# Kernel tuning notes

Hardware: AMD Instinct MI355X
Metric: run time of the kernel (lower is better)

The kernel has to match this reference:

```python
import math
import jax, jax.numpy as jnp
import numpy as np
from jax import lax

# Exact mod-2^32 addition requires float64 accumulation (as the torch code does).
jax.config.update("jax_enable_x64", True)

MD5_K = [int(2 ** 32 * abs(math.sin(i + 1))) & 0xFFFFFFFF for i in range(64)]
MD5_S = [7, 12, 17, 22] * 4 + [5, 9, 14, 20] * 4 + [4, 11, 16, 23] * 4 + [6, 10, 15, 21] * 4
NUM_ROUNDS = 64
NUM_BLOCKS = 2
_XOR_GRAD_SCALE = 0.5

def _int_to_bits(n, width=32):
    return np.array([(n >> i) & 1 for i in range(width)], dtype=np.float32)

K_BITS = np.stack([_int_to_bits(k) for k in MD5_K])          # (64, 32) LSB-first
H0 = _int_to_bits(1732584193)
H1 = _int_to_bits(4023233417)
H2 = _int_to_bits(2562383102)
H3 = _int_to_bits(271733878)
_pad_bytes = [128] + [0] * 55 + [0, 2, 0, 0, 0, 0, 0, 0]
PAD_BITS = np.array([(bv >> j) & 1 for bv in _pad_bytes for j in range(8)], dtype=np.float32)  # (512,)
POWERS = 2.0 ** np.arange(32, dtype=np.float64)              # (32,)

def soft_xor(a, b):
    return a + b - 2 * a * b

def soft_and(a, b):
    return a * b

def soft_or(a, b):
    return a + b - a * b

def soft_not(a):
    return 1 - a

def soft_leftrotate(x, n):
    # cat([x[..., -n:], x[..., :-n]]) == roll by +n along last axis
    return jnp.roll(x, n, axis=-1)

def _hard_add(a, b):
    # Exact addition mod 2^32 via float64; hard bits, no gradient path.
    p = jnp.asarray(POWERS)
    a_val = (a.astype(jnp.float64) * p).sum(axis=-1, keepdims=True)
    b_val = (b.astype(jnp.float64) * p).sum(axis=-1, keepdims=True)
    s = jnp.fmod(a_val + b_val, 2.0 ** 32)
    return jnp.floor(jnp.fmod(s / p, 2.0)).astype(a.dtype)

def soft_add32(a, b):
    # Forward exact, backward XOR straight-through (STE_MODE == 'xor').
    hard = _hard_add(a, b)
    proxy = soft_xor(a, b) * _XOR_GRAD_SCALE
    return lax.stop_gradient(hard) + proxy - lax.stop_gradient(proxy)

def _compress(a, b, c, d, words, K):
    # words: (B, 16, 32); a,b,c,d: (B, 32)
    for i in range(NUM_ROUNDS):
        if i < 16:
            f = soft_or(soft_and(b, c), soft_and(soft_not(b), d))
            g = i
        elif i < 32:
            f = soft_or(soft_and(d, b), soft_and(soft_not(d), c))
            g = (5 * i + 1) % 16
        elif i < 48:
            f = soft_xor(soft_xor(b, c), d)
            g = (3 * i + 5) % 16
        else:
            f = soft_xor(c, soft_or(b, soft_not(d)))
            g = (7 * i) % 16
        f = soft_add32(f, a)
        f = soft_add32(f, jnp.broadcast_to(K[i], a.shape))
        f = soft_add32(f, words[..., g, :])
        a, d, c = d, c, b
        b = soft_add32(b, soft_leftrotate(f, MD5_S[i]))
    return a, b, c, d

def setup_inputs() -> dict:
    key = jax.random.key(0)
    B = 131072
    message_bits = jax.random.uniform(key, (B, 512), dtype=jnp.float32)
    return {"message_bits": message_bits}

def reference(message_bits) -> jnp.ndarray:
    B = message_bits.shape[0]
    K = jnp.asarray(K_BITS)
    words1 = message_bits.reshape(B, 16, 32)
    a = jnp.broadcast_to(jnp.asarray(H0), (B, 32)).astype(message_bits.dtype)
    b = jnp.broadcast_to(jnp.asarray(H1), (B, 32)).astype(message_bits.dtype)
    c = jnp.broadcast_to(jnp.asarray(H2), (B, 32)).astype(message_bits.dtype)
    d = jnp.broadcast_to(jnp.asarray(H3), (B, 32)).astype(message_bits.dtype)
    da, db, dc, dd = _compress(a, b, c, d, words1, K)
    a = soft_add32(a, da)
    b = soft_add32(b, db)
    c = soft_add32(c, dc)
    d = soft_add32(d, dd)
    if NUM_BLOCKS >= 2:
        words2 = jnp.broadcast_to(jnp.asarray(PAD_BITS), (B, 512)).reshape(B, 16, 32).astype(message_bits.dtype)
        da, db, dc, dd = _compress(a, b, c, d, words2, K)
        a = soft_add32(a, da)
        b = soft_add32(b, db)
        c = soft_add32(c, dc)
        d = soft_add32(d, dd)
    return jnp.concatenate([a, b, c, d], axis=-1)  # (B, 128)
```

## Files before the change

kernel.cpp:

```cpp
#include <hip/hip_runtime.h>
#include <stdint.h>
#include <stddef.h>

#pragma clang fp contract(off)

typedef unsigned int u32;
typedef unsigned long long u64;


__device__ __forceinline__ u32 rotl32(u32 x, u32 n) {
    return (x << n) | (x >> (32u - n));
}

#define WF   0x1.fffffep-1f
#define TWOW 0x1.fffffep+0f

__device__ __forceinline__ u32 dirty0(float y) {
#pragma clang fp contract(off)
    float p = 0.5f * y;
    float t = 1.0f + p;
    return (u32)((t - p) != 1.0f);
}
__device__ __forceinline__ u32 dirty1(float y) {
#pragma clang fp contract(off)
    float u = 1.0f + y;
    float v = y + y;
    float xr = u - v;
    float p = 0.5f * xr;
    float t = 1.0f + p;
    return (u32)((t - p) != 1.0f);
}
__device__ __forceinline__ u32 dirtyw(float y) {
#pragma clang fp contract(off)
    float u = WF + y;
    float v = TWOW * y;
    float xr = u - v;
    float p = 0.5f * xr;
    float t = 1.0f + p;
    return (u32)((t - p) != 1.0f);
}

__device__ __forceinline__ double sum_packed(u32 h, u32 d) {
#pragma clang fp contract(off)
    double s = fma((double)(d & 0x1FFFFFFFu), -0x1p-24,
                   (double)(h & 0x1FFFFFFFu));
    int n29 = (int)(((h >> 29) & 1u) << 24) - (int)((d >> 29) & 1u);
    s = fma((double)n29, 0x1p5, s);
    int n30 = (int)(((h >> 30) & 1u) << 24) - (int)((d >> 30) & 1u);
    s = fma((double)n30, 0x1p6, s);
    int n31 = (int)((h >> 31) << 24) - (int)(d >> 31);
    s = fma((double)n31, 0x1p7, s);
    return s;
}

struct Planes { u32 Mh, QA, QB, QC, Re, mO, mWW2, mU; };

__device__ __forceinline__ Planes classes(int type, u32 Bh, u32 Bd,
                                          u32 Ch, u32 Cd, u32 Dh, u32 Dd) {
    Planes P;
    if (type <= 1) {
        u32 selh, seld, mainh, maind, subh, subd;
        if (type == 0) { selh=Bh; seld=Bd; mainh=Ch; maind=Cd; subh=Dh; subd=Dd; }
        else           { selh=Dh; seld=Dd; mainh=Bh; maind=Bd; subh=Ch; subd=Cd; }
        u32 selZ = ~selh, selO = selh & ~seld;
        u32 mainO = mainh & ~maind, subO = subh & ~subd;
        u32 mO  = (selZ & subO) | (selO & mainO);
        u32 mW  = (selZ & subd) | (selO & maind) | (seld & mainO);
        u32 mW2 = seld & maind;
        u32 tse = seld & ~mainh;
        u32 mTE = tse & subh;
        u32 mE  = tse & subd;
        P.mO = mO; P.mU = 0u;
        P.mWW2 = mW | mW2;
        P.Mh = mO | P.mWW2;
        P.QA = mW | mTE;
        P.QB = P.mWW2;
        P.QC = ~P.mWW2;
        P.Re = mE;
    } else if (type == 2) {
        u32 BZ=~Bh, CZ=~Ch, DZ=~Dh;
        u32 BO=Bh&~Bd, CO=Ch&~Cd, DO=Dh&~Dd;
        u32 x1Z = (BZ&CZ)|(BO&CO);
        u32 x1O = (BZ&CO)|(BO&CZ);
        u32 x1W = (BZ&Cd)|(Bd&CZ);
        u32 x1U = (Bh&Cd)|(Bd&Ch);
        u32 mO  = (x1Z&DO)|(x1O&DZ);
        u32 mW  = (x1Z&Dd)|(x1W&DZ);
        u32 mU  = (x1O&Dd)|(x1W&Dh)|(x1U&DZ);
        u32 mW2 = x1U&DO;
        u32 mW4 = x1U&Dd;
        P.mO = mO; P.mU = mU;
        P.mWW2 = mW | mW2;
        P.Mh = mO | mW | mW2 | mW4;
        P.QA = mW;
        P.QB = mW2 | mW | mU;
        P.QC = ~(mW | mW2 | mW4);
        P.Re = 0u;
    } else {
        u32 BZ=~Bh, CZ=~Ch, DZ=~Dh;
        u32 BO=Bh&~Bd, CO=Ch&~Cd, DO=Dh&~Dd;
        u32 oZ = BZ & DO;
        u32 oO = (BZ&DZ) | (BO&~Dd) | (Bd&DZ);
        u32 oW = (BO&Dd) | (Bd&Dh);
        u32 oT = BZ & Dd;
        u32 mO  = (CZ&oO)|(CO&oZ);
        u32 mW  = (CZ&oW)|(Cd&oZ);
        u32 mT  = CZ&oT;
        u32 mU  = (CO&oW)|(Cd&(oO|oW));
        u32 mW2 = Ch&oT;
        P.mO = mO; P.mU = mU;
        P.mWW2 = mW | mW2;
        P.Mh = mO | mW | mW2;
        P.QA = mW | mT;
        P.QB = mW2 | mW | mU;
        P.QC = ~(mW | mW2);
        P.Re = 0u;
    }
    return P;
}

__device__ __forceinline__ double vbit(const Planes& P, int k) {
#pragma clang fp contract(off)
    u32 hb = (P.Mh >> k) & 1u;
    u32 n = (hb << 24) + ((P.QA >> k) & 1u) + (((P.QB >> k) & 1u) << 1)
          + (((P.QC >> k) & 1u) << 2);
    double cd = ((P.Re >> k) & 1u) ? (-0x1p-22 - 0x1p-48) : -0x1p-22;
    return fma((double)n, 0x1p-24, cd);
}

__device__ __forceinline__ double chain_slow(const Planes& P) {
#pragma clang fp contract(off)
    double accF = 0.0;
    #pragma unroll
    for (int k = 0; k < 32; ++k)
        accF = fma(vbit(P, k), (double)(1u << k), accF);
    return accF;
}

__device__ __forceinline__ double chain_fast(const Planes& P) {
#pragma clang fp contract(off)
    const u32 M29 = 0x1FFFFFFFu;
    u32 lo = (P.QA & M29) + ((P.QB & M29) << 1) + ((P.QC & M29) << 2);
    u64 I = (((u64)(P.Mh & M29)) << 24) + (u64)lo - 0x7FFFFFFCull;
    double X = fma((double)(u32)(I >> 32), 0x1p32, (double)(u32)I);
    double accF = X * 0x1p-24;
    accF = fma(vbit(P, 29), 0x1p29, accF);
    accF = fma(vbit(P, 30), 0x1p30, accF);
    accF = fma(vbit(P, 31), 0x1p31, accF);
    return accF;
}

__device__ const u32 Ku[64] = {
    0xd76aa478u,0xe8c7b756u,0x242070dbu,0xc1bdceeeu,
    0xf57c0fafu,0x4787c62au,0xa8304613u,0xfd469501u,
    0x698098d8u,0x8b44f7afu,0xffff5bb1u,0x895cd7beu,
    0x6b901122u,0xfd987193u,0xa679438eu,0x49b40821u,
    0xf61e2562u,0xc040b340u,0x265e5a51u,0xe9b6c7aau,
    0xd62f105du,0x02441453u,0xd8a1e681u,0xe7d3fbc8u,
    0x21e1cde6u,0xc33707d6u,0xf4d50d87u,0x455a14edu,
    0xa9e3e905u,0xfcefa3f8u,0x676f02d9u,0x8d2a4c8au,
    0xfffa3942u,0x8771f681u,0x6d9d6122u,0xfde5380cu,
    0xa4beea44u,0x4bdecfa9u,0xf6bb4b60u,0xbebfbc70u,
    0x289b7ec6u,0xeaa127fau,0xd4ef3085u,0x04881d05u,
    0xd9d4d039u,0xe6db99e5u,0x1fa27cf8u,0xc4ac5665u,
    0xf4292244u,0x432aff97u,0xab9423a7u,0xfc93a039u,
    0x655b59c3u,0x8f0ccc92u,0xffeff47du,0x85845dd1u,
    0x6fa87e4fu,0xfe2ce6e0u,0xa3014314u,0x4e0811a1u,
    0xf7537e82u,0xbd3af235u,0x2ad7d2bbu,0xeb86d391u
};
__device__ const u32 Stab[64] = {
    7,12,17,22, 7,12,17,22, 7,12,17,22, 7,12,17,22,
    5, 9,14,20, 5, 9,14,20, 5, 9,14,20, 5, 9,14,20,
    4,11,16,23, 4,11,16,23, 4,11,16,23, 4,11,16,23,
    6,10,15,21, 6,10,15,21, 6,10,15,21, 6,10,15,21
};
__device__ const u32 PWt[16] = { 128u,0,0,0, 0,0,0,0, 0,0,0,0, 0,0,512u,0 };

#define ROUND(TYPE, i, g)                                                     \
    {                                                                         \
        Planes P = classes(TYPE, Bh, Bd, Ch, Cd, Dh, Dd);                     \
        u32 df1 = (P.mO & Ad) | (P.mWW2 & Ah) | (P.mU & ~Ah);                 \
        double accF;                                                          \
        if (TYPE >= 2) {                                                      \
            accF = chain_fast(P);                                             \
        } else if (__ballot((P.Re & 0x1FFFFFFFu) != 0u) == 0ull) {            \
            accF = chain_fast(P);                                             \
        } else {                                                              \
            accF = chain_slow(P);                                             \
        }                                                                     \
        double s1 = accF + vA; if (s1 >= 0x1p32) s1 -= 0x1p32;                \
        u32 h1 = (u32)s1, d1 = h1 & df1;                                      \
        double V1 = sum_packed(h1, d1);                                       \
        u32 Kv = Ku[i];                                                       \
        double s2 = V1 + (double)Kv; if (s2 >= 0x1p32) s2 -= 0x1p32;          \
        u32 h2 = (u32)s2, d2 = h2 & d1 & Kv;                                  \
        double V2 = sum_packed(h2, d2);                                       \
        u32 df3; double bv;                                                   \
        if (blk == 0) {                                                       \
            df3 = (~h2 & lds_d0[g][tid]) | ((h2 & ~d2) & lds_d1[g][tid])      \
                | (d2 & lds_dw[g][tid]);                                      \
            bv = lds_wv[g][tid];                                              \
        } else {                                                              \
            u32 pw = PWt[g];                                                  \
            df3 = d2 & pw;                                                    \
            bv = (double)pw;                                                  \
        }                                                                     \
        double s3 = V2 + bv; if (s3 >= 0x1p32) s3 -= 0x1p32;                  \
        u32 h3 = (u32)s3, d3 = h3 & df3;                                      \
        u32 sh = Stab[i];                                                     \
        u32 rh = rotl32(h3, sh), rd = rotl32(d3, sh);                         \
        double Vr = sum_packed(rh, rd);                                       \
        double s4 = vB + Vr; if (s4 >= 0x1p32) s4 -= 0x1p32;                  \
        u32 h4 = (u32)s4;                                                     \
        u32 d4 = h4 & (Bh & rh) & (Bd | rd);                                  \
        double V4 = sum_packed(h4, d4);                                       \
        Ah = Dh; Ad = Dd; vA = vD;                                            \
        Dh = Ch; Dd = Cd; vD = vC;                                            \
        Ch = Bh; Cd = Bd; vC = vB;                                            \
        Bh = h4; Bd = d4; vB = V4;                                            \
    }

__global__ __launch_bounds__(128, 2) void softmd5_kernel(
    const float* __restrict__ msg, float* __restrict__ out, int B)
{
#pragma clang fp contract(off)
    __shared__ double lds_wv[16][128];
    __shared__ u32 lds_d0[16][128];
    __shared__ u32 lds_d1[16][128];
    __shared__ u32 lds_dw[16][128];

    const int tid = threadIdx.x;
    const int e = blockIdx.x * 128 + tid;
    if (e >= B) return;

    const float* row = msg + (size_t)e * 512;
    const float4* r4 = reinterpret_cast<const float4*>(row);

    for (int w = 0; w < 16; ++w) {
        double acc = 0.0;
        u32 m0 = 0, m1 = 0, mw = 0;
        #pragma unroll
        for (int q = 0; q < 8; ++q) {
            float4 v = r4[w * 8 + q];
            const int k = 4 * q;
            acc = fma((double)v.x, (double)(1u << (k + 0)), acc);
            acc = fma((double)v.y, (double)(1u << (k + 1)), acc);
            acc = fma((double)v.z, (double)(1u << (k + 2)), acc);
            acc = fma((double)v.w, (double)(1u << (k + 3)), acc);
            m0 |= dirty0(v.x) << (k+0); m0 |= dirty0(v.y) << (k+1);
            m0 |= dirty0(v.z) << (k+2); m0 |= dirty0(v.w) << (k+3);
            m1 |= dirty1(v.x) << (k+0); m1 |= dirty1(v.y) << (k+1);
            m1 |= dirty1(v.z) << (k+2); m1 |= dirty1(v.w) << (k+3);
            mw |= dirtyw(v.x) << (k+0); mw |= dirtyw(v.y) << (k+1);
            mw |= dirtyw(v.z) << (k+2); mw |= dirtyw(v.w) << (k+3);
        }
        lds_wv[w][tid] = acc;
        lds_d0[w][tid] = m0;
        lds_d1[w][tid] = m1;
        lds_dw[w][tid] = mw;
    }

    u32 Ah = 0x67452301u, Ad = 0u;
    u32 Bh = 0xefcdab89u, Bd = 0u;
    u32 Ch = 0x98badcfeu, Cd = 0u;
    u32 Dh = 0x10325476u, Dd = 0u;
    double vA = (double)Ah, vB = (double)Bh, vC = (double)Ch, vD = (double)Dh;

    #pragma unroll
    for (int blk = 0; blk < 2; ++blk) {
        const u32 sAh=Ah, sAd=Ad, sBh=Bh, sBd=Bd;
        const u32 sCh=Ch, sCd=Cd, sDh=Dh, sDd=Dd;
        const double sVA=vA, sVB=vB, sVC=vC, sVD=vD;

        #pragma unroll 1
        for (int i = 0; i < 16; ++i) ROUND(0, i, i)
        #pragma unroll 1
        for (int i = 16; i < 32; ++i) ROUND(1, i, (5 * i + 1) & 15)
        #pragma unroll 1
        for (int i = 32; i < 48; ++i) ROUND(2, i, (3 * i + 5) & 15)
        #pragma unroll 1
        for (int i = 48; i < 64; ++i) ROUND(3, i, (7 * i) & 15)

        {
            double s = sVA + vA; if (s >= 0x1p32) s -= 0x1p32;
            u32 h = (u32)s; u32 dd = h & (sAh & Ah) & (sAd | Ad);
            Ah = h; Ad = dd; vA = sum_packed(Ah, Ad);
        }
        {
            double s = sVB + vB; if (s >= 0x1p32) s -= 0x1p32;
            u32 h = (u32)s; u32 dd = h & (sBh & Bh) & (sBd | Bd);
            Bh = h; Bd = dd; vB = sum_packed(Bh, Bd);
        }
        {
            double s = sVC + vC; if (s >= 0x1p32) s -= 0x1p32;
            u32 h = (u32)s; u32 dd = h & (sCh & Ch) & (sCd | Cd);
            Ch = h; Cd = dd; vC = sum_packed(Ch, Cd);
        }
        {
            double s = sVD + vD; if (s >= 0x1p32) s -= 0x1p32;
            u32 h = (u32)s; u32 dd = h & (sDh & Dh) & (sDd | Dd);
            Dh = h; Dd = dd; vD = sum_packed(Dh, Dd);
        }
    }

    float4* orow = reinterpret_cast<float4*>(out) + (size_t)e * 32;
    const u32 H[4] = {Ah, Bh, Ch, Dh};
    #pragma unroll
    for (int hh = 0; hh < 4; ++hh) {
        #pragma unroll
        for (int q = 0; q < 8; ++q) {
            float4 v;
            v.x = (float)((H[hh] >> (q * 4 + 0)) & 1u);
            v.y = (float)((H[hh] >> (q * 4 + 1)) & 1u);
            v.z = (float)((H[hh] >> (q * 4 + 2)) & 1u);
            v.w = (float)((H[hh] >> (q * 4 + 3)) & 1u);
            orow[hh * 8 + q] = v;
        }
    }
}

extern "C" void kernel_launch(void* const* d_in, const int* in_sizes, int n_in,
                              void* d_out, int out_size, void* d_ws, size_t ws_size,
                              hipStream_t stream) {
    (void)n_in; (void)d_ws; (void)ws_size; (void)out_size;
    const float* msg = (const float*)d_in[0];
    float* out = (float*)d_out;
    const int B = in_sizes[0] / 512;
    const int block = 128;
    const int grid = (B + block - 1) / block;
    softmd5_kernel<<<grid, block, 0, stream>>>(msg, out, B);
}
```

Measured before the change: 501.4 us.

## Switch second block to plain integer MD5 once all lanes are clean

Splits the unrolled two-block loop into separate first and second compression passes. In the second block, once a wavefront-wide ballot shows no dirty bits remain in A-D, rounds run as plain 32-bit integer MD5 instead of the double-precision soft emulation. The slow chain path is also reworked to compute the clean low bits in one integer step up to the first dirty bit, then loop only over the remaining bits. This trades extra code size and per-round ballot checks for much cheaper rounds when state becomes exact, and relies on the integer path being bit-identical to the emulated path for clean values.

New measurement: 478.8 us. 1.05x faster.

```diff
diff --git a/kernel.cpp b/kernel.cpp
--- a/kernel.cpp
+++ b/kernel.cpp
@@ -128,13 +128,17 @@
     return fma((double)n, 0x1p-24, cd);
 }
 
-__device__ __forceinline__ double chain_slow(const Planes& P) {
-#pragma clang fp contract(off)
-    double accF = 0.0;
-    #pragma unroll
-    for (int k = 0; k < 32; ++k)
-        accF = fma(vbit(P, k), (double)(1u << k), accF);
-    return accF;
+__device__ double chain_slow(const Planes& P) {
+#pragma clang fp contract(off)
+    u32 ReL = P.Re & 0x1FFFFFFFu;
+    int kE = (ReL == 0u) ? 29 : __builtin_ctz(ReL);
+    u32 pm = (1u << kE) - 1u;
+    u32 lo = (P.QA & pm) + ((P.QB & pm) << 1) + ((P.QC & pm) << 2);
+    u64 I = (((u64)(P.Mh & pm)) << 24) + (u64)lo - ((4ull << kE) - 4ull);
+    double S = fma((double)(u32)(I >> 32), 0x1p32, (double)(u32)I) * 0x1p-24;
+    for (int k = kE; k < 32; ++k)
+        S = fma(vbit(P, k), (double)(1u << k), S);
+    return S;
 }
 
 __device__ __forceinline__ double chain_fast(const Planes& P) {
@@ -176,7 +180,7 @@
 };
 __device__ const u32 PWt[16] = { 128u,0,0,0, 0,0,0,0, 0,0,0,0, 0,0,512u,0 };
 
-#define ROUND(TYPE, i, g)                                                     \
+#define ROUND(TYPE, WSEL, i, g)                                               \
     {                                                                         \
         Planes P = classes(TYPE, Bh, Bd, Ch, Cd, Dh, Dd);                     \
         u32 df1 = (P.mO & Ad) | (P.mWW2 & Ah) | (P.mU & ~Ah);                 \
@@ -196,7 +200,7 @@
         u32 h2 = (u32)s2, d2 = h2 & d1 & Kv;                                  \
         double V2 = sum_packed(h2, d2);                                       \
         u32 df3; double bv;                                                   \
-        if (blk == 0) {                                                       \
+        if (WSEL == 0) {                                                      \
             df3 = (~h2 & lds_d0[g][tid]) | ((h2 & ~d2) & lds_d1[g][tid])      \
                 | (d2 & lds_dw[g][tid]);                                      \
             bv = lds_wv[g][tid];                                              \
@@ -220,6 +224,25 @@
         Bh = h4; Bd = d4; vB = V4;                                            \
     }
 
+#define INTROUND(TYPE, i, g)                                                  \
+    {                                                                         \
+        u32 f;                                                                \
+        if (TYPE == 0)      f = (Bh & Ch) | (~Bh & Dh);                       \
+        else if (TYPE == 1) f = (Dh & Bh) | (~Dh & Ch);                       \
+        else if (TYPE == 2) f = Bh ^ Ch ^ Dh;                                 \
+        else                f = Ch ^ (Bh | ~Dh);                              \
+        f += Ah + Ku[i] + PWt[g];                                             \
+        u32 nb = Bh + rotl32(f, Stab[i]);                                     \
+        Ah = Dh; Dh = Ch; Ch = Bh; Bh = nb;                                   \
+    }
+
+#define B1ROUND(TYPE, i, g)                                                   \
+    {                                                                         \
+        if (!intm) intm = (__ballot((Ad | Bd | Cd | Dd) != 0u) == 0ull);      \
+        if (intm) INTROUND(TYPE, i, g)                                        \
+        else      ROUND(TYPE, 1, i, g)                                        \
+    }
+
 __global__ __launch_bounds__(128, 2) void softmd5_kernel(
     const float* __restrict__ msg, float* __restrict__ out, int B)
 {
@@ -266,20 +289,19 @@
     u32 Dh = 0x10325476u, Dd = 0u;
     double vA = (double)Ah, vB = (double)Bh, vC = (double)Ch, vD = (double)Dh;
 
-    #pragma unroll
-    for (int blk = 0; blk < 2; ++blk) {
+    {
         const u32 sAh=Ah, sAd=Ad, sBh=Bh, sBd=Bd;
         const u32 sCh=Ch, sCd=Cd, sDh=Dh, sDd=Dd;
         const double sVA=vA, sVB=vB, sVC=vC, sVD=vD;
 
         #pragma unroll 1
-        for (int i = 0; i < 16; ++i) ROUND(0, i, i)
-        #pragma unroll 1
-        for (int i = 16; i < 32; ++i) ROUND(1, i, (5 * i + 1) & 15)
-        #pragma unroll 1
-        for (int i = 32; i < 48; ++i) ROUND(2, i, (3 * i + 5) & 15)
-        #pragma unroll 1
-        for (int i = 48; i < 64; ++i) ROUND(3, i, (7 * i) & 15)
+        for (int i = 0; i < 16; ++i) ROUND(0, 0, i, i)
+        #pragma unroll 1
+        for (int i = 16; i < 32; ++i) ROUND(1, 0, i, (5 * i + 1) & 15)
+        #pragma unroll 1
+        for (int i = 32; i < 48; ++i) ROUND(2, 0, i, (3 * i + 5) & 15)
+        #pragma unroll 1
+        for (int i = 48; i < 64; ++i) ROUND(3, 0, i, (7 * i) & 15)
 
         {
             double s = sVA + vA; if (s >= 0x1p32) s -= 0x1p32;
@@ -300,6 +322,47 @@
             double s = sVD + vD; if (s >= 0x1p32) s -= 0x1p32;
             u32 h = (u32)s; u32 dd = h & (sDh & Dh) & (sDd | Dd);
             Dh = h; Dd = dd; vD = sum_packed(Dh, Dd);
+        }
+    }
+
+    {
+        const u32 sAh=Ah, sAd=Ad, sBh=Bh, sBd=Bd;
+        const u32 sCh=Ch, sCd=Cd, sDh=Dh, sDd=Dd;
+        const double sVA=vA, sVB=vB, sVC=vC, sVD=vD;
+        bool intm = false;
+
+        #pragma unroll 1
+        for (int i = 0; i < 16; ++i) B1ROUND(0, i, i)
+        #pragma unroll 1
+        for (int i = 16; i < 32; ++i) B1ROUND(1, i, (5 * i + 1) & 15)
+        #pragma unroll 1
+        for (int i = 32; i < 48; ++i) B1ROUND(2, i, (3 * i + 5) & 15)
+        #pragma unroll 1
+        for (int i = 48; i < 64; ++i) B1ROUND(3, i, (7 * i) & 15)
+
+        if (intm) {
+            vA = (double)Ah; vB = (double)Bh; vC = (double)Ch; vD = (double)Dh;
+        }
+
+        {
+            double s = sVA + vA; if (s >= 0x1p32) s -= 0x1p32;
+            u32 h = (u32)s; u32 dd = h & (sAh & Ah) & (sAd | Ad);
+            Ah = h; Ad = dd;
+        }
+        {
+            double s = sVB + vB; if (s >= 0x1p32) s -= 0x1p32;
+            u32 h = (u32)s; u32 dd = h & (sBh & Bh) & (sBd | Bd);
+            Bh = h; Bd = dd;
+        }
+        {
+            double s = sVC + vC; if (s >= 0x1p32) s -= 0x1p32;
+            u32 h = (u32)s; u32 dd = h & (sCh & Ch) & (sCd | Cd);
+            Ch = h; Cd = dd;
+        }
+        {
+            double s = sVD + vD; if (s >= 0x1p32) s -= 0x1p32;
+            u32 h = (u32)s; u32 dd = h & (sDh & Dh) & (sDd | Dd);
+            Dh = h; Dd = dd;
         }
     }
 
```
